# Kernel optimization log

Measured on AMD Instinct MI355X. Metric: run time of the kernel, lower is better.

The kernel has to match this reference:

```python
import jax, jax.numpy as jnp
import numpy as np

B, CIN, COUT, SDIM, RES, K = 8, 512, 512, 512, 64, 3
AFF_SCALE = 1.0 / np.sqrt(SDIM)          # LinearAct: 1/sqrt(in_features)
CONV_SCALE = 1.0 / np.sqrt(CIN * K * K)  # ModulatedConv2d: 1/sqrt(in*k*k)
LRELU_GAIN = np.sqrt(2.0)                # bias_act 'lrelu' default gain


def setup_inputs() -> dict:
    key = jax.random.key(0)
    k = jax.random.split(key, 5)
    x = jax.random.normal(k[0], (B, CIN, RES, RES), dtype=jnp.float32)
    w = jax.random.normal(k[1], (B, SDIM), dtype=jnp.float32)
    noise = jax.random.normal(k[2], (B, 1, RES, RES), dtype=jnp.float32)
    affine_w = jax.random.normal(k[3], (CIN, SDIM), dtype=jnp.float32)
    affine_b = jnp.ones((CIN,), dtype=jnp.float32)          # bias.data.fill_(1.0)
    conv_w = jax.random.normal(k[4], (COUT, CIN, K, K), dtype=jnp.float32)
    noise_scale = jnp.asarray(0.1, dtype=jnp.float32)        # InjectNoise.scale (nonzero for a meaningful test)
    bias = jnp.zeros((COUT,), dtype=jnp.float32)
    return {"x": x, "w": w, "noise": noise, "affine_w": affine_w,
            "affine_b": affine_b, "conv_w": conv_w,
            "noise_scale": noise_scale, "bias": bias}


def reference(x, w, noise, affine_w, affine_b, conv_w, noise_scale, bias):
    # affine (LinearAct, act='linear'): style = w @ (W*scale)^T + b
    style = jnp.einsum('bs,cs->bc', w, affine_w * AFF_SCALE) + affine_b  # [B, CIN]

    # modulate + demodulate: per-sample weight [B, COUT, CIN, K, K]
    wt = conv_w[None] * style[:, None, :, None, None] * CONV_SCALE
    d = jax.lax.rsqrt(jnp.sum(wt * wt, axis=(2, 3, 4), keepdims=True) + 1e-8)
    wt = wt * d

    # grouped conv (groups=B) == per-sample conv; flip_weight=True -> plain correlation
    def conv_one(xi, wi):
        return jax.lax.conv_general_dilated(
            xi[None], wi, window_strides=(1, 1), padding=[(1, 1), (1, 1)],
            dimension_numbers=('NCHW', 'OIHW', 'NCHW'))[0]

    y = jax.vmap(conv_one)(x, wt)  # [B, COUT, RES, RES]

    # noise -> bias -> lrelu(0.2) * sqrt(2)
    y = y + noise * noise_scale
    y = jax.nn.leaky_relu(y + bias[None, :, None, None], 0.2) * LRELU_GAIN
    return y
```

## Files before the change

kernel.cpp:

```cpp
#include <hip/hip_runtime.h>
#include <hip/hip_bf16.h>

typedef unsigned short u16;

#define BATCH 8
#define CIN 512
#define COUT 512
#define SDIM 512
#define RES 64
#define PIX (RES * RES)
#define NKT 72

__device__ __constant__ static const float kAffScale  = 0.04419417382415922f;
__device__ __constant__ static const float kConvScale = 0.014731391274719742f;
__device__ __constant__ static const float kGain      = 1.4142135623730951f;

typedef __bf16 bf16x8 __attribute__((ext_vector_type(8)));
typedef float  f32x4  __attribute__((ext_vector_type(4)));

__global__ void style_k(const float* __restrict__ w, const float* __restrict__ aw,
                        const float* __restrict__ ab, float* __restrict__ style,
                        float* __restrict__ zbuf) {
  int tid = blockIdx.x * 256 + threadIdx.x;
  if (blockIdx.x == 0 && threadIdx.x < 64) zbuf[threadIdx.x] = 0.0f;
  int b = tid >> 9, c = tid & 511;
  const float* wp = w + b * SDIM;
  const float* ap = aw + c * SDIM;
  float s = 0.0f;
  for (int k = 0; k < SDIM; ++k) s += wp[k] * ap[k];
  style[tid] = s * kAffScale + ab[c];
}

__global__ void cw2_k(const float* __restrict__ cw, float* __restrict__ cw2) {
  int tid = blockIdx.x * 256 + threadIdx.x;
  const float* p = cw + tid * 9;
  float s = 0.0f;
  #pragma unroll
  for (int t = 0; t < 9; ++t) { float v = p[t]; s += v * v; }
  cw2[tid] = s;
}

__global__ void fac_k(const float* __restrict__ style, const float* __restrict__ cw2,
                      float* __restrict__ fac) {
  int wid  = blockIdx.x * 4 + (threadIdx.x >> 6);
  int lane = threadIdx.x & 63;
  int b = wid >> 9, o = wid & 511;
  const float* st = style + b * CIN;
  const float* c2 = cw2 + o * CIN;
  float s = 0.0f;
  for (int i = lane; i < CIN; i += 64) { float sv = st[i]; s += sv * sv * c2[i]; }
  #pragma unroll
  for (int off = 32; off; off >>= 1) s += __shfl_xor(s, off);
  if (lane == 0) {
    float d = rsqrtf(s * kConvScale * kConvScale + 1e-8f);
    fac[wid] = d * kConvScale;
  }
}

__global__ void wcast_k(const float* __restrict__ cw, u16* __restrict__ wb) {
  int tid = blockIdx.x * 256 + threadIdx.x;
  int o = tid >> 9, i = tid & 511;
  const float* p = cw + tid * 9;
  #pragma unroll
  for (int t = 0; t < 9; ++t) {
    __hip_bfloat16 h = __float2bfloat16(p[t]);
    wb[(t * COUT + o) * CIN + i] = *(u16*)&h;
  }
}

__global__ void modx_k(const float* __restrict__ x, const float* __restrict__ style,
                       u16* __restrict__ xs) {
  __shared__ float t[64][65];
  int b  = blockIdx.z;
  int it = blockIdx.y * 64;
  int pt = blockIdx.x * 64;
  int tp = threadIdx.x & 63;
  int tr = threadIdx.x >> 6;
  for (int r = tr; r < 64; r += 4) {
    int i = it + r;
    t[r][tp] = x[(b * CIN + i) * PIX + pt + tp] * style[b * CIN + i];
  }
  __syncthreads();
  for (int r = tr; r < 64; r += 4) {
    __hip_bfloat16 h = __float2bfloat16(t[tp][r]);
    xs[(size_t)(b * PIX + pt + r) * CIN + it + tp] = *(u16*)&h;
  }
}

__launch_bounds__(512, 2)
__global__ void gemm_k(const u16* __restrict__ wb, const u16* __restrict__ xs,
                       const float* __restrict__ fac, const float* __restrict__ noise,
                       const float* __restrict__ nscale_p, const float* __restrict__ bias,
                       const float* __restrict__ zbuf, float* __restrict__ y) {
  __shared__ __align__(16) u16 Abuf[2][16384];
  __shared__ __align__(16) u16 Bbuf[2][16384];

  const int tid = threadIdx.x;
  const int bid = blockIdx.x;
  const int swz = (bid & 7) * 32 + (bid >> 3);
  const int mt = swz >> 7;
  const int nt = swz & 127;
  const int b  = nt >> 4;
  const int pimg  = (nt & 15) * 256;
  const int hbase = pimg >> 6;

  const int lane = tid & 63;
  const int wv = tid >> 6;
  const int wm = wv >> 2;
  const int wn = wv & 3;
  const int l15 = lane & 15, l4 = lane >> 4;
  const int slot = (l4 ^ ((l15 >> 1) & 3)) * 8;

  const int sg8 = (((tid & 3) ^ ((tid >> 3) & 3)) << 3);
  size_t offA[2]; int hr[2], wc[2];
  #pragma unroll
  for (int p = 0; p < 2; ++p) {
    int row = (p * 512 + tid) >> 2;
    offA[p] = (size_t)(mt * 256 + row) * CIN + sg8;
    hr[p] = hbase + (row >> 6);
    wc[p] = row & 63;
  }

  auto stA = [&](int ktx, int kh) {
    if (ktx >= NKT) ktx -= NKT;
    const int tap = ktx >> 3;
    const int i0  = (ktx & 7) << 6;
    const int d   = ktx & 1;
    const u16* basep = wb + (size_t)tap * (COUT * CIN) + i0 + kh * 32;
    #pragma unroll
    for (int p = 0; p < 2; ++p) {
      const u16* src = basep + offA[p];
      __builtin_amdgcn_global_load_lds(
          (const __attribute__((address_space(1))) void*)src,
          (__attribute__((address_space(3))) void*)(&Abuf[d][kh * 8192 + (p * 512 + tid) * 8]),
          16, 0, 0);
    }
  };
  auto stB = [&](int ktx, int kh) {
    if (ktx >= NKT) ktx -= NKT;
    const int tap = ktx >> 3;
    const int i0  = (ktx & 7) << 6;
    const int dy  = tap < 3 ? -1 : (tap < 6 ? 0 : 1);
    const int dx  = (tap - (tap < 3 ? 0 : (tap < 6 ? 3 : 6))) - 1;
    const int d   = ktx & 1;
    #pragma unroll
    for (int p = 0; p < 2; ++p) {
      int hh = hr[p] + dy, ww = wc[p] + dx;
      const u16* src = ((unsigned)hh < 64u && (unsigned)ww < 64u)
          ? xs + ((size_t)(b * PIX + hh * 64 + ww) * CIN + i0 + kh * 32 + sg8)
          : (const u16*)zbuf;
      __builtin_amdgcn_global_load_lds(
          (const __attribute__((address_space(1))) void*)src,
          (__attribute__((address_space(3))) void*)(&Bbuf[d][kh * 8192 + (p * 512 + tid) * 8]),
          16, 0, 0);
    }
  };

  f32x4 acc[8][4];
  #pragma unroll
  for (int i = 0; i < 8; ++i)
    #pragma unroll
    for (int j = 0; j < 4; ++j) acc[i][j] = (f32x4){0.f, 0.f, 0.f, 0.f};

  stA(0, 0); stB(0, 0); stA(0, 1); stB(0, 1); stA(1, 0); stB(1, 0);
  asm volatile("s_waitcnt vmcnt(8)" ::: "memory");
  __builtin_amdgcn_s_barrier();

#define LDA(mi, kh) (*(const bf16x8*)&Ab[(kh) * 8192 + (wm * 128 + (mi) * 16 + l15) * 32 + slot])
#define LDB(ni, kh) (*(const bf16x8*)&Bb[(kh) * 8192 + (wn * 64 + (ni) * 16 + l15) * 32 + slot])

  for (int kt = 0; kt < NKT; ++kt) {
    const u16* Ab = &Abuf[kt & 1][0];
    const u16* Bb = &Bbuf[kt & 1][0];
    bf16x8 bfr[4], af[4];

    #pragma unroll
    for (int ni = 0; ni < 4; ++ni) bfr[ni] = LDB(ni, 0);
    #pragma unroll
    for (int j = 0; j < 4; ++j) af[j] = LDA(j, 0);
    stA(kt + 1, 1);
    __builtin_amdgcn_s_barrier();
    asm volatile("s_waitcnt lgkmcnt(0)" ::: "memory");
    __builtin_amdgcn_sched_barrier(0);
    __builtin_amdgcn_s_setprio(1);
    #pragma unroll
    for (int j = 0; j < 4; ++j)
      #pragma unroll
      for (int ni = 0; ni < 4; ++ni)
        acc[j][ni] = __builtin_amdgcn_mfma_f32_16x16x32_bf16(af[j], bfr[ni], acc[j][ni], 0, 0, 0);
    __builtin_amdgcn_s_setprio(0);
    __builtin_amdgcn_s_barrier();

    #pragma unroll
    for (int j = 0; j < 4; ++j) af[j] = LDA(4 + j, 0);
    stB(kt + 1, 1);
    __builtin_amdgcn_s_barrier();
    asm volatile("s_waitcnt lgkmcnt(0)" ::: "memory");
    __builtin_amdgcn_sched_barrier(0);
    __builtin_amdgcn_s_setprio(1);
    #pragma unroll
    for (int j = 0; j < 4; ++j)
      #pragma unroll
      for (int ni = 0; ni < 4; ++ni)
        acc[4 + j][ni] = __builtin_amdgcn_mfma_f32_16x16x32_bf16(af[j], bfr[ni], acc[4 + j][ni], 0, 0, 0);
    __builtin_amdgcn_s_setprio(0);
    asm volatile("s_waitcnt vmcnt(8)" ::: "memory");
    __builtin_amdgcn_s_barrier();

    #pragma unroll
    for (int ni = 0; ni < 4; ++ni) bfr[ni] = LDB(ni, 1);
    #pragma unroll
    for (int j = 0; j < 4; ++j) af[j] = LDA(j, 1);
    stA(kt + 2, 0);
    __builtin_amdgcn_s_barrier();
    asm volatile("s_waitcnt lgkmcnt(0)" ::: "memory");
    __builtin_amdgcn_sched_barrier(0);
    __builtin_amdgcn_s_setprio(1);
    #pragma unroll
    for (int j = 0; j < 4; ++j)
      #pragma unroll
      for (int ni = 0; ni < 4; ++ni)
        acc[j][ni] = __builtin_amdgcn_mfma_f32_16x16x32_bf16(af[j], bfr[ni], acc[j][ni], 0, 0, 0);
    __builtin_amdgcn_s_setprio(0);
    __builtin_amdgcn_s_barrier();

    #pragma unroll
    for (int j = 0; j < 4; ++j) af[j] = LDA(4 + j, 1);
    stB(kt + 2, 0);
    __builtin_amdgcn_s_barrier();
    asm volatile("s_waitcnt lgkmcnt(0)" ::: "memory");
    __builtin_amdgcn_sched_barrier(0);
    __builtin_amdgcn_s_setprio(1);
    #pragma unroll
    for (int j = 0; j < 4; ++j)
      #pragma unroll
      for (int ni = 0; ni < 4; ++ni)
        acc[4 + j][ni] = __builtin_amdgcn_mfma_f32_16x16x32_bf16(af[j], bfr[ni], acc[4 + j][ni], 0, 0, 0);
    __builtin_amdgcn_s_setprio(0);
    asm volatile("s_waitcnt vmcnt(8)" ::: "memory");
    __builtin_amdgcn_s_barrier();
  }
#undef LDA
#undef LDB

  const float ns = nscale_p[0];
  float nz[4];
  #pragma unroll
  for (int ni = 0; ni < 4; ++ni) {
    int pix = pimg + wn * 64 + ni * 16 + l15;
    nz[ni] = noise[b * PIX + pix] * ns;
  }
  #pragma unroll
  for (int mi = 0; mi < 8; ++mi) {
    int o = mt * 256 + wm * 128 + mi * 16 + l4 * 4;
    f32x4 fv = *(const f32x4*)&fac[b * COUT + o];
    f32x4 bv = *(const f32x4*)&bias[o];
    #pragma unroll
    for (int r = 0; r < 4; ++r) {
      float* yp = y + (size_t)(b * COUT + o + r) * PIX + pimg + wn * 64 + l15;
      #pragma unroll
      for (int ni = 0; ni < 4; ++ni) {
        float v = acc[mi][ni][r] * fv[r] + nz[ni] + bv[r];
        v = (v > 0.0f ? v : 0.2f * v) * kGain;
        yp[ni * 16] = v;
      }
    }
  }
}

extern "C" void kernel_launch(void* const* d_in, const int* in_sizes, int n_in,
                              void* d_out, int out_size, void* d_ws, size_t ws_size,
                              hipStream_t stream) {
  const float* x      = (const float*)d_in[0];
  const float* w      = (const float*)d_in[1];
  const float* noise  = (const float*)d_in[2];
  const float* aff_w  = (const float*)d_in[3];
  const float* aff_b  = (const float*)d_in[4];
  const float* conv_w = (const float*)d_in[5];
  const float* nscale = (const float*)d_in[6];
  const float* bias   = (const float*)d_in[7];
  float* y = (float*)d_out;

  char* ws = (char*)d_ws;
  float* style = (float*)(ws);
  float* fac   = (float*)(ws + 16384);
  float* cw2   = (float*)(ws + 32768);
  float* zbuf  = (float*)(ws + 1081344);
  u16*   wb    = (u16*)(ws + 1081600);
  u16*   xs    = (u16*)(ws + 5800192);

  style_k<<<16, 256, 0, stream>>>(w, aff_w, aff_b, style, zbuf);
  cw2_k<<<1024, 256, 0, stream>>>(conv_w, cw2);
  fac_k<<<1024, 256, 0, stream>>>(style, cw2, fac);
  wcast_k<<<1024, 256, 0, stream>>>(conv_w, wb);
  modx_k<<<dim3(64, 8, 8), 256, 0, stream>>>(x, style, xs);
  gemm_k<<<256, 512, 0, stream>>>(wb, xs, fac, noise, nscale, bias, zbuf, y);
}
```

Before: 200.0 us.

## Relayout weights and activations into 32-channel panels for contiguous tile loads

The bf16 weight and modulated-activation buffers are rewritten in a panel-major layout: each 32-channel slice is stored contiguously per tap or per image. Each k-step's global-to-LDS loads therefore read compact 64-byte rows inside one panel instead of striding across the full 512-channel row, with simpler address arithmetic. The explicit lgkmcnt waits and sched_barriers before each MFMA block are also removed, leaving the compiler free to interleave LDS reads with MFMAs. The cost is a strided, less coalesced write pattern in the preprocessing kernels, plus reliance on compiler-inserted waits for the LDS fragments.

```diff
diff --git a/kernel.cpp b/kernel.cpp
--- a/kernel.cpp
+++ b/kernel.cpp
@@ -57,19 +57,19 @@
   }
 }
 
-__global__ void wcast_k(const float* __restrict__ cw, u16* __restrict__ wb) {
+__global__ void wcast_k(const float* __restrict__ cw, u16* __restrict__ wbt) {
   int tid = blockIdx.x * 256 + threadIdx.x;
   int o = tid >> 9, i = tid & 511;
   const float* p = cw + tid * 9;
   #pragma unroll
   for (int t = 0; t < 9; ++t) {
     __hip_bfloat16 h = __float2bfloat16(p[t]);
-    wb[(t * COUT + o) * CIN + i] = *(u16*)&h;
+    wbt[((size_t)(t * 16 + (i >> 5)) * 512 + o) * 32 + (i & 31)] = *(u16*)&h;
   }
 }
 
 __global__ void modx_k(const float* __restrict__ x, const float* __restrict__ style,
-                       u16* __restrict__ xs) {
+                       u16* __restrict__ xst) {
   __shared__ float t[64][65];
   int b  = blockIdx.z;
   int it = blockIdx.y * 64;
@@ -81,14 +81,16 @@
     t[r][tp] = x[(b * CIN + i) * PIX + pt + tp] * style[b * CIN + i];
   }
   __syncthreads();
+  int i = it + tp;
+  size_t base = ((size_t)(b * 16 + (i >> 5)) * PIX) * 32 + (i & 31);
   for (int r = tr; r < 64; r += 4) {
     __hip_bfloat16 h = __float2bfloat16(t[tp][r]);
-    xs[(size_t)(b * PIX + pt + r) * CIN + it + tp] = *(u16*)&h;
+    xst[base + (size_t)(pt + r) * 32] = *(u16*)&h;
   }
 }
 
 __launch_bounds__(512, 2)
-__global__ void gemm_k(const u16* __restrict__ wb, const u16* __restrict__ xs,
+__global__ void gemm_k(const u16* __restrict__ wbt, const u16* __restrict__ xst,
                        const float* __restrict__ fac, const float* __restrict__ noise,
                        const float* __restrict__ nscale_p, const float* __restrict__ bias,
                        const float* __restrict__ zbuf, float* __restrict__ y) {
@@ -111,25 +113,24 @@
   const int l15 = lane & 15, l4 = lane >> 4;
   const int slot = (l4 ^ ((l15 >> 1) & 3)) * 8;
 
-  const int sg8 = (((tid & 3) ^ ((tid >> 3) & 3)) << 3);
-  size_t offA[2]; int hr[2], wc[2];
+  const int sgE = ((tid & 3) ^ ((tid >> 3) & 3)) << 3;
+  int aoff[2], boff[2], hr[2], wc[2];
   #pragma unroll
   for (int p = 0; p < 2; ++p) {
     int row = (p * 512 + tid) >> 2;
-    offA[p] = (size_t)(mt * 256 + row) * CIN + sg8;
+    aoff[p] = (mt * 256 + row) * 32 + sgE;
+    boff[p] = (pimg + row) * 32 + sgE;
     hr[p] = hbase + (row >> 6);
     wc[p] = row & 63;
   }
 
   auto stA = [&](int ktx, int kh) {
     if (ktx >= NKT) ktx -= NKT;
-    const int tap = ktx >> 3;
-    const int i0  = (ktx & 7) << 6;
-    const int d   = ktx & 1;
-    const u16* basep = wb + (size_t)tap * (COUT * CIN) + i0 + kh * 32;
+    const int d = ktx & 1;
+    const u16* pan = wbt + ((size_t)((ktx >> 3) * 16 + ((ktx & 7) << 1) + kh) << 14);
     #pragma unroll
     for (int p = 0; p < 2; ++p) {
-      const u16* src = basep + offA[p];
+      const u16* src = pan + aoff[p];
       __builtin_amdgcn_global_load_lds(
           (const __attribute__((address_space(1))) void*)src,
           (__attribute__((address_space(3))) void*)(&Abuf[d][kh * 8192 + (p * 512 + tid) * 8]),
@@ -139,16 +140,16 @@
   auto stB = [&](int ktx, int kh) {
     if (ktx >= NKT) ktx -= NKT;
     const int tap = ktx >> 3;
-    const int i0  = (ktx & 7) << 6;
     const int dy  = tap < 3 ? -1 : (tap < 6 ? 0 : 1);
     const int dx  = (tap - (tap < 3 ? 0 : (tap < 6 ? 3 : 6))) - 1;
     const int d   = ktx & 1;
+    const u16* pan = xst + ((size_t)(b * 16 + ((ktx & 7) << 1) + kh) << 17);
+    const int shiftE = (dy * 64 + dx) * 32;
     #pragma unroll
     for (int p = 0; p < 2; ++p) {
       int hh = hr[p] + dy, ww = wc[p] + dx;
       const u16* src = ((unsigned)hh < 64u && (unsigned)ww < 64u)
-          ? xs + ((size_t)(b * PIX + hh * 64 + ww) * CIN + i0 + kh * 32 + sg8)
-          : (const u16*)zbuf;
+          ? pan + (boff[p] + shiftE) : (const u16*)zbuf;
       __builtin_amdgcn_global_load_lds(
           (const __attribute__((address_space(1))) void*)src,
           (__attribute__((address_space(3))) void*)(&Bbuf[d][kh * 8192 + (p * 512 + tid) * 8]),
@@ -180,8 +181,6 @@
     for (int j = 0; j < 4; ++j) af[j] = LDA(j, 0);
     stA(kt + 1, 1);
     __builtin_amdgcn_s_barrier();
-    asm volatile("s_waitcnt lgkmcnt(0)" ::: "memory");
-    __builtin_amdgcn_sched_barrier(0);
     __builtin_amdgcn_s_setprio(1);
     #pragma unroll
     for (int j = 0; j < 4; ++j)
@@ -195,8 +194,6 @@
     for (int j = 0; j < 4; ++j) af[j] = LDA(4 + j, 0);
     stB(kt + 1, 1);
     __builtin_amdgcn_s_barrier();
-    asm volatile("s_waitcnt lgkmcnt(0)" ::: "memory");
-    __builtin_amdgcn_sched_barrier(0);
     __builtin_amdgcn_s_setprio(1);
     #pragma unroll
     for (int j = 0; j < 4; ++j)
@@ -213,8 +210,6 @@
     for (int j = 0; j < 4; ++j) af[j] = LDA(j, 1);
     stA(kt + 2, 0);
     __builtin_amdgcn_s_barrier();
-    asm volatile("s_waitcnt lgkmcnt(0)" ::: "memory");
-    __builtin_amdgcn_sched_barrier(0);
     __builtin_amdgcn_s_setprio(1);
     #pragma unroll
     for (int j = 0; j < 4; ++j)
@@ -228,8 +223,6 @@
     for (int j = 0; j < 4; ++j) af[j] = LDA(4 + j, 1);
     stB(kt + 2, 0);
     __builtin_amdgcn_s_barrier();
-    asm volatile("s_waitcnt lgkmcnt(0)" ::: "memory");
-    __builtin_amdgcn_sched_barrier(0);
     __builtin_amdgcn_s_setprio(1);
     #pragma unroll
     for (int j = 0; j < 4; ++j)
@@ -286,13 +279,13 @@
   float* fac   = (float*)(ws + 16384);
   float* cw2   = (float*)(ws + 32768);
   float* zbuf  = (float*)(ws + 1081344);
-  u16*   wb    = (u16*)(ws + 1081600);
-  u16*   xs    = (u16*)(ws + 5800192);
+  u16*   wbt   = (u16*)(ws + 1081600);
+  u16*   xst   = (u16*)(ws + 5800192);
 
   style_k<<<16, 256, 0, stream>>>(w, aff_w, aff_b, style, zbuf);
   cw2_k<<<1024, 256, 0, stream>>>(conv_w, cw2);
   fac_k<<<1024, 256, 0, stream>>>(style, cw2, fac);
-  wcast_k<<<1024, 256, 0, stream>>>(conv_w, wb);
-  modx_k<<<dim3(64, 8, 8), 256, 0, stream>>>(x, style, xs);
-  gemm_k<<<256, 512, 0, stream>>>(wb, xs, fac, noise, nscale, bias, zbuf, y);
-}
+  wcast_k<<<1024, 256, 0, stream>>>(conv_w, wbt);
+  modx_k<<<dim3(64, 8, 8), 256, 0, stream>>>(x, style, xst);
+  gemm_k<<<256, 512, 0, stream>>>(wbt, xst, fac, noise, nscale, bias, zbuf, y);
+}
```

Measured after the change: 231.6 us. 1.16x slower.
